# Kernel tuning notes

Measured on AMD Instinct MI355X. Metric: run time of the kernel, lower is better.

The kernel has to match this reference:

```python
import jax, jax.numpy as jnp
import numpy as np

N_ITEMS = 50000
N_USERS = 20000
N_NODES = N_ITEMS + N_USERS
D = 128
N_REL = 3
NNZ = 800000
K_LAYERS = 2
B, S, L = 256, 4, 50


def setup_inputs() -> dict:
    key = jax.random.key(0)
    ks = iter(jax.random.split(key, 40))
    stdv = float(1.0 / np.sqrt(D))

    def uni(shape):
        return jax.random.uniform(next(ks), shape, jnp.float32, -stdv, stdv)

    id_emb = (jax.random.normal(next(ks), (N_ITEMS, D), jnp.float32) * 0.1).at[0].set(0.0)  # padding_idx=0
    user_emb = jax.random.normal(next(ks), (N_USERS, D), jnp.float32) * 0.1
    inp = dict(
        id_emb=id_emb, user_emb=user_emb,
        lin_r_w=uni((K_LAYERS, N_REL, D, D)),
        upi_w=uni((K_LAYERS, D, D)), upi_b=uni((K_LAYERS, D)),
        upu_w=uni((K_LAYERS, D, D)), upu_b=uni((K_LAYERS, D)),
        w_ih=uni((3 * D, 2 * D)), w_hh=uni((3 * D, D)),
        b_ih=uni((3 * D,)), b_hh=uni((3 * D,)),
        b_iah=uni((D,)), b_oah=uni((D,)),
        ei_w=uni((D, D)), ei_b=uni((D,)),
        eo_w=uni((D, D)), eo_b=uni((D,)),
        q1_w=uni((D, D)), q2_w=uni((D, D)), att_w=uni((D,)),
        fuse_w=uni((D, 2 * D)), fuse_b=uni((D,)),
    )
    # global heterogeneous graph: COO per relation over item+user nodes
    inp['rel_rows'] = jax.random.randint(next(ks), (N_REL, NNZ), 0, N_NODES, dtype=jnp.int32)
    inp['rel_cols'] = jax.random.randint(next(ks), (N_REL, NNZ), 0, N_NODES, dtype=jnp.int32)
    inp['rel_vals'] = jax.random.uniform(next(ks), (N_REL, NNZ), jnp.float32) * 0.1
    # session batch: every session has length in [2, L]
    lens = jax.random.randint(next(ks), (B, S), 2, L + 1)
    raw = jax.random.randint(next(ks), (B, S, L), 1, N_ITEMS)
    inp['ids'] = (raw * (jnp.arange(L)[None, None, :] < lens[:, :, None])).astype(jnp.int32)
    inp['uid'] = jax.random.randint(next(ks), (B,), 0, N_USERS, dtype=jnp.int32)
    inp['u_type'] = jax.random.randint(next(ks), (B,), 0, 3).astype(jnp.float32)
    return inp


def _hgnn(h_item, h_user, rel_rows, rel_cols, rel_vals, lin_r_w, upi_w, upi_b, upu_w, upu_b):
    Ni = h_item.shape[0]
    N = Ni + h_user.shape[0]
    for k in range(lin_r_w.shape[0]):
        h_all = jnp.concatenate([h_item, h_user], 0)
        msg = jnp.zeros_like(h_all)
        for r in range(rel_rows.shape[0]):
            Wh = h_all @ lin_r_w[k, r].T  # per-relation linear
            msg = msg + jax.ops.segment_sum(Wh[rel_cols[r]] * rel_vals[r][:, None],
                                            rel_rows[r], num_segments=N)  # sparse.mm
        h_item = jax.nn.relu((msg[:Ni] + h_item) @ upi_w[k].T + upi_b[k])
        h_user = jax.nn.relu((msg[Ni:] + h_user) @ upu_w[k].T + upu_b[k])
    return h_item, h_user


def reference(id_emb, user_emb, lin_r_w, upi_w, upi_b, upu_w, upu_b,
              w_ih, w_hh, b_ih, b_hh, b_iah, b_oah,
              ei_w, ei_b, eo_w, eo_b, q1_w, q2_w, att_w, fuse_w, fuse_b,
              rel_rows, rel_cols, rel_vals, ids, uid, u_type):
    Bb, Ss, Ll = ids.shape
    N = Ss * Bb
    ids_sb = jnp.transpose(ids, (1, 0, 2)).reshape(N, Ll)  # session-major, matches torch concat order
    lens = (ids_sb != 0).sum(-1)  # >= 2 by construction -> all sessions valid
    rows = jnp.arange(N)
    target = ids_sb[rows, lens - 1]
    Lp = Ll - 1
    m_in = jnp.arange(Lp)[None, :] < (lens - 1)[:, None]
    seq_in = ids_sb[:, :Lp] * m_in
    # session graph: consecutive-item edges; in-half sub-diagonal, out-half super-diagonal
    valid = (m_in[:, 1:] & m_in[:, :-1]).astype(jnp.float32)  # [N, Lp-1]
    i1 = jnp.arange(1, Lp)
    i0 = jnp.arange(Lp - 1)
    a_in = jnp.zeros((N, Lp, Lp), jnp.float32).at[:, i1, i0].set(valid)
    a_out = jnp.zeros((N, Lp, Lp), jnp.float32).at[:, i0, i1].set(valid)
    deg = jnp.clip(a_in.sum(-1), 1.0, None)[..., None]
    a_in = a_in / deg
    a_out = a_out / deg
    h = id_emb[seq_in]  # [N, Lp, D]
    # SessionGNN GRU-style cell (step=1)
    m_i = jnp.matmul(a_in, h @ ei_w.T + ei_b) + b_iah
    m_o = jnp.matmul(a_out, h @ eo_w.T + eo_b) + b_oah
    gi = jnp.concatenate([m_i, m_o], -1) @ w_ih.T + b_ih
    gh = h @ w_hh.T + b_hh
    i_r, i_i, i_n = jnp.split(gi, 3, -1)
    h_r, h_i, h_n = jnp.split(gh, 3, -1)
    rg = jax.nn.sigmoid(i_r + h_r)
    zg = jax.nn.sigmoid(i_i + h_i)
    ng = jnp.tanh(i_n + rg * h_n)
    h = ng + zg * (h - ng)
    # attention readout
    ht = h[rows, jnp.clip(lens - 2, 0, None)]
    alpha = jax.nn.sigmoid((ht @ q1_w.T)[:, None, :] + h @ q2_w.T) @ att_w  # [N, Lp]
    alpha = alpha * m_in.astype(jnp.float32)
    alpha = alpha / (alpha.sum(1, keepdims=True) + 1e-8)
    c_cur = jnp.einsum('nl,nld->nd', alpha, h)
    # global HGNN user context
    g_item, g_user = _hgnn(id_emb[:N_ITEMS], user_emb[:N_USERS], rel_rows, rel_cols,
                           rel_vals, lin_r_w, upi_w, upi_b, upu_w, upu_b)
    c_hist = g_user[jnp.tile(uid, Ss)]
    reps = jnp.concatenate([c_cur, c_hist], -1) @ fuse_w.T + fuse_b
    return reps, target, jnp.tile(u_type, Ss)
```

## Files before the change

### kernel.cpp

```cpp
#include <hip/hip_runtime.h>
#include <hip/hip_bf16.h>

typedef __hip_bfloat16 bf16;
typedef unsigned int uint32;
typedef __attribute__((ext_vector_type(8))) short short8;
typedef __attribute__((ext_vector_type(4))) float f32x4;

#define N_ITEMS_C 50000
#define N_USERS_C 20000
#define N_NODES_C 70000
#define NNZ_C 800000
#define NSESS 1024
#define LP 49
#define NTOK (NSESS * LP)
#define NBK 137

__device__ __forceinline__ float bflo(uint32 u) { return __uint_as_float(u << 16); }
__device__ __forceinline__ float bfhi(uint32 u) { return __uint_as_float(u & 0xffff0000u); }
__device__ __forceinline__ uint32 packbf(float a, float b) {
    return (uint32)__bfloat16_as_ushort(__float2bfloat16(a)) |
           ((uint32)__bfloat16_as_ushort(__float2bfloat16(b)) << 16);
}

__global__ void init_hab_kernel(const float2* __restrict__ idp, const float2* __restrict__ usp,
                                uint32* __restrict__ hab) {
    int i = blockIdx.x * 256 + threadIdx.x;
    float2 w = (i < 3200000) ? idp[i] : usp[i - 3200000];
    hab[i] = packbf(w.x, w.y);
}

__global__ __launch_bounds__(256) void bucket_hist_kernel(
    const int* __restrict__ rel_rows, int* __restrict__ bhist)
{
    __shared__ int hist[NBK];
    const int r = blockIdx.y, tid = threadIdx.x;
    if (tid < NBK) hist[tid] = 0;
    __syncthreads();
    const int* rr = rel_rows + (size_t)r * NNZ_C;
#pragma unroll
    for (int i = 0; i < 16; ++i) {
        int e = blockIdx.x * 4096 + i * 256 + tid;
        if (e < NNZ_C) atomicAdd(&hist[rr[e] >> 9], 1);
    }
    __syncthreads();
    if (tid < NBK && hist[tid]) atomicAdd(&bhist[r * NBK + tid], hist[tid]);
}

__global__ __launch_bounds__(256) void bucket_scan_kernel(
    const int* __restrict__ bhist, int* __restrict__ bbase)
{
    __shared__ int s[256];
    const int tid = threadIdx.x;
    for (int r = 0; r < 3; ++r) {
        s[tid] = (tid < NBK) ? bhist[r * NBK + tid] : 0;
        __syncthreads();
        for (int d = 1; d < 256; d <<= 1) {
            int t = (tid >= d) ? s[tid - d] : 0;
            __syncthreads();
            s[tid] += t;
            __syncthreads();
        }
        if (tid < NBK) bbase[r * (NBK + 1) + tid + 1] = s[tid];
        if (tid == 0) bbase[r * (NBK + 1)] = 0;
        __syncthreads();
    }
}

__global__ __launch_bounds__(256) void bucket_scatter_kernel(
    const int* __restrict__ rel_rows, const int* __restrict__ rel_cols,
    const float* __restrict__ rel_vals, const int* __restrict__ bbase,
    int* __restrict__ cursor, int2* __restrict__ tmp)
{
    __shared__ int hist[NBK], gbase[NBK], cur2[NBK];
    const int r = blockIdx.y, tid = threadIdx.x;
    if (tid < NBK) { hist[tid] = 0; cur2[tid] = 0; }
    __syncthreads();
    const int* rr = rel_rows + (size_t)r * NNZ_C;
    const int* rc = rel_cols + (size_t)r * NNZ_C;
    const float* rv = rel_vals + (size_t)r * NNZ_C;
#pragma unroll
    for (int i = 0; i < 16; ++i) {
        int e = blockIdx.x * 4096 + i * 256 + tid;
        if (e < NNZ_C) atomicAdd(&hist[rr[e] >> 9], 1);
    }
    __syncthreads();
    if (tid < NBK)
        gbase[tid] = bbase[r * (NBK + 1) + tid] +
                     (hist[tid] ? atomicAdd(&cursor[r * NBK + tid], hist[tid]) : 0);
    __syncthreads();
    int2* tp = tmp + (size_t)r * NNZ_C;
#pragma unroll
    for (int i = 0; i < 16; ++i) {
        int e = blockIdx.x * 4096 + i * 256 + tid;
        if (e < NNZ_C) {
            int row = rr[e];
            int bk = row >> 9;
            int rank = atomicAdd(&cur2[bk], 1);
            uint32 fb = __float_as_uint(rv[e]);
            uint32 pk = (uint32)rc[e] | (((fb >> 16) & 0x7FFFu) << 17);
            tp[gbase[bk] + rank] = make_int2((int)pk, row);
        }
    }
}

__global__ __launch_bounds__(256) void bucket_refine_kernel(
    const int2* __restrict__ tmp, const int* __restrict__ bbase,
    int* __restrict__ offs, uint32* __restrict__ edges)
{
    __shared__ int cnt[512], offsL[512], cur[512];
    __shared__ uint32 outb[6656];
    const int b = blockIdx.x, r = blockIdx.y, tid = threadIdx.x;
    const int lane = tid & 63, wid = tid >> 6;
    const int row0 = b << 9;
    const int e0 = bbase[r * (NBK + 1) + b];
    const int e1 = bbase[r * (NBK + 1) + b + 1];
    cnt[tid] = 0; cnt[256 + tid] = 0; cur[tid] = 0; cur[256 + tid] = 0;
    __syncthreads();
    const int2* tp = tmp + (size_t)r * NNZ_C;
    for (int e = e0 + tid; e < e1; e += 256)
        atomicAdd(&cnt[tp[e].y - row0], 1);
    __syncthreads();
    if (wid == 0) {
        int carry = 0;
        for (int c = 0; c < 8; ++c) {
            int x = cnt[c * 64 + lane];
            int inc = x;
#pragma unroll
            for (int d = 1; d < 64; d <<= 1) {
                int y = __shfl_up(inc, d, 64);
                if (lane >= d) inc += y;
            }
            offsL[c * 64 + lane] = inc - x + carry;
            carry += __shfl(inc, 63, 64);
        }
    }
    __syncthreads();
    for (int i = tid; i < 512; i += 256) {
        int row = row0 + i;
        if (row < 70001) offs[(size_t)r * 70001 + row] = e0 + offsL[i];
    }
    for (int e = e0 + tid; e < e1; e += 256) {
        int2 E = tp[e];
        int lr_ = E.y - row0;
        int slot = offsL[lr_] + atomicAdd(&cur[lr_], 1);
        if (slot < 6656) outb[slot] = (uint32)E.x;
    }
    __syncthreads();
    uint32* eo = edges + (size_t)r * NNZ_C + e0;
    for (int i = tid; i < e1 - e0; i += 256) eo[i] = outb[i];
}

__global__ __launch_bounds__(256) void gather_kernel(
    const uint32* __restrict__ hab, const uint32* __restrict__ edges,
    const int* __restrict__ offs, uint32* __restrict__ T)
{
    const int r = blockIdx.y;
    const int row = blockIdx.x * 4 + (threadIdx.x >> 6);
    const int lane = threadIdx.x & 63;
    const uint32* __restrict__ ed = edges + (size_t)r * NNZ_C;
    const int* __restrict__ of = offs + (size_t)r * 70001;
    int e0 = of[row], e1 = of[row + 1];
    float ax = 0.f, ay = 0.f;
    int e = e0;
    for (; e + 4 <= e1; e += 4) {
        uint32 E0 = ed[e], E1 = ed[e + 1], E2 = ed[e + 2], E3 = ed[e + 3];
        uint32 u0 = hab[(size_t)(E0 & 0x1FFFFu) * 64 + lane];
        uint32 u1 = hab[(size_t)(E1 & 0x1FFFFu) * 64 + lane];
        uint32 u2 = hab[(size_t)(E2 & 0x1FFFFu) * 64 + lane];
        uint32 u3 = hab[(size_t)(E3 & 0x1FFFFu) * 64 + lane];
        float v0 = __uint_as_float((E0 >> 1) & 0x7FFF0000u);
        float v1 = __uint_as_float((E1 >> 1) & 0x7FFF0000u);
        float v2 = __uint_as_float((E2 >> 1) & 0x7FFF0000u);
        float v3 = __uint_as_float((E3 >> 1) & 0x7FFF0000u);
        ax += v0 * bflo(u0) + v1 * bflo(u1) + v2 * bflo(u2) + v3 * bflo(u3);
        ay += v0 * bfhi(u0) + v1 * bfhi(u1) + v2 * bfhi(u2) + v3 * bfhi(u3);
    }
    for (; e < e1; ++e) {
        uint32 E = ed[e];
        uint32 u = hab[(size_t)(E & 0x1FFFFu) * 64 + lane];
        float v = __uint_as_float((E >> 1) & 0x7FFF0000u);
        ax += v * bflo(u); ay += v * bfhi(u);
    }
    T[(size_t)row * 192 + r * 64 + lane] = packbf(ax, ay);
}

__global__ __launch_bounds__(256, 3) void wprep_kernel(
    const float* __restrict__ upi_w, const float* __restrict__ upu_w,
    const float* __restrict__ lin_r_w, int k, uint32* __restrict__ Wcat)
{
    __shared__ float As[128][65];
    __shared__ __align__(8) bf16 Ws[128][66];
    const int which = blockIdx.y, seg = which / 3, r = which % 3;
    const float* U  = (seg == 0 ? upi_w : upu_w) + (size_t)k * 16384;
    const float* Wr = lin_r_w + (size_t)(k * 3 + r) * 16384;
    uint32* out = Wcat + (size_t)seg * 32768;
    const int tid = threadIdx.x;
    const int row0 = blockIdx.x * 64;
#pragma unroll
    for (int i = 0; i < 8; ++i) {
        int id = i * 256 + tid;
        int rr = id >> 5, c4 = (id & 31) << 2;
        float4 v = *(const float4*)&U[(size_t)(row0 + rr) * 128 + c4];
        As[c4][rr] = v.x; As[c4+1][rr] = v.y; As[c4+2][rr] = v.z; As[c4+3][rr] = v.w;
    }
    const int m0 = (tid & 15) * 4;
    const int n0 = (tid >> 4) * 8;
    float acc[4][8];
#pragma unroll
    for (int i = 0; i < 4; ++i)
#pragma unroll
        for (int j = 0; j < 8; ++j) acc[i][j] = 0.f;
    for (int p = 0; p < 2; ++p) {
        if (p) __syncthreads();
        for (int i = 0; i < 32; ++i) {
            int id = i * 256 + tid;
            int c = id >> 6, kf = id & 63;
            Ws[c][kf] = __float2bfloat16(Wr[(size_t)(p * 64 + kf) * 128 + c]);
        }
        __syncthreads();
        for (int k2 = 0; k2 < 32; ++k2) {
            int kk = p * 64 + 2 * k2;
            float av0[4], av1[4];
#pragma unroll
            for (int i = 0; i < 4; ++i) { av0[i] = As[kk][m0 + i]; av1[i] = As[kk + 1][m0 + i]; }
#pragma unroll
            for (int j = 0; j < 8; ++j) {
                uint32 wp = *(const uint32*)&Ws[n0 + j][2 * k2];
                float w0 = bflo(wp), w1 = bfhi(wp);
#pragma unroll
                for (int i = 0; i < 4; ++i)
                    acc[i][j] = fmaf(av1[i], w1, fmaf(av0[i], w0, acc[i][j]));
            }
        }
    }
#pragma unroll
    for (int i = 0; i < 4; ++i) {
        int n = row0 + m0 + i;
#pragma unroll
        for (int j = 0; j < 8; j += 2)
            out[(size_t)n * 256 + (r * 128 + n0 + j) / 2] = packbf(acc[i][j], acc[i][j + 1]);
    }
}

__global__ __launch_bounds__(256) void upack_kernel(
    const float* __restrict__ upi_w, const float* __restrict__ upu_w,
    int k, uint32* __restrict__ Wcat)
{
    int id = blockIdx.x * 256 + threadIdx.x;
    int seg = id >> 13, p = id & 8191;
    int n = p >> 6, j2 = (p & 63);
    const float* U = (seg ? upu_w : upi_w) + (size_t)k * 16384;
    float2 w = *(const float2*)&U[(size_t)n * 128 + j2 * 2];
    Wcat[(size_t)seg * 32768 + (size_t)n * 256 + 192 + j2] = packbf(w.x, w.y);
}

__global__ __launch_bounds__(256) void hgnn_update_mfma_kernel(
    const bf16* __restrict__ T, uint32* __restrict__ hab,
    const bf16* __restrict__ Wcat, const float* __restrict__ bias, int row0, int M)
{
    const int tid = threadIdx.x;
    const int wv = tid >> 6, lane = tid & 63, quad = lane >> 4, lr = lane & 15;
    const int rbase = blockIdx.x * 64;
    const bf16* hb = (const bf16*)hab;
    f32x4 acc[4][2];
#pragma unroll
    for (int mt = 0; mt < 4; ++mt) { acc[mt][0] = (f32x4){0,0,0,0}; acc[mt][1] = (f32x4){0,0,0,0}; }
    int arow[4];
#pragma unroll
    for (int mt = 0; mt < 4; ++mt) {
        int rr = rbase + mt * 16 + lr;
        arow[mt] = row0 + (rr < M ? rr : M - 1);
    }
#pragma unroll
    for (int ks = 0; ks < 16; ++ks) {
        short8 b0 = *(const short8*)&Wcat[(size_t)(wv * 32 + lr) * 512 + ks * 32 + quad * 8];
        short8 b1 = *(const short8*)&Wcat[(size_t)(wv * 32 + 16 + lr) * 512 + ks * 32 + quad * 8];
#pragma unroll
        for (int mt = 0; mt < 4; ++mt) {
            short8 a;
            if (ks < 12) a = *(const short8*)&T[(size_t)arow[mt] * 384 + ks * 32 + quad * 8];
            else         a = *(const short8*)&hb[(size_t)arow[mt] * 128 + (ks - 12) * 32 + quad * 8];
            acc[mt][0] = __builtin_amdgcn_mfma_f32_16x16x32_bf16(a, b0, acc[mt][0], 0, 0, 0);
            acc[mt][1] = __builtin_amdgcn_mfma_f32_16x16x32_bf16(a, b1, acc[mt][1], 0, 0, 0);
        }
    }
    __syncthreads();
    unsigned short* hw = (unsigned short*)hab;
#pragma unroll
    for (int s = 0; s < 2; ++s) {
        int col = wv * 32 + s * 16 + lr;
        float bv = bias[col];
#pragma unroll
        for (int mt = 0; mt < 4; ++mt)
#pragma unroll
            for (int reg = 0; reg < 4; ++reg) {
                int rr = rbase + mt * 16 + quad * 4 + reg;
                if (rr < M) {
                    float v = fmaxf(acc[mt][s][reg] + bv, 0.f);
                    hw[(size_t)(row0 + rr) * 128 + col] = __bfloat16_as_ushort(__float2bfloat16(v));
                }
            }
    }
}

__global__ __launch_bounds__(256) void mfma_nt_kernel(
    const bf16* __restrict__ A, const int* __restrict__ rowmap,
    const bf16* __restrict__ W0, const bf16* __restrict__ W1,
    const float* __restrict__ b0, const float* __restrict__ b1,
    float* __restrict__ O0, float* __restrict__ O1, int M)
{
    const int tid = threadIdx.x;
    const int wv = tid >> 6, lane = tid & 63, quad = lane >> 4, lr = lane & 15;
    const int rbase = blockIdx.x * 64;
    int arow[4];
#pragma unroll
    for (int mt = 0; mt < 4; ++mt) {
        int rr = rbase + mt * 16 + lr;
        rr = rr < M ? rr : M - 1;
        arow[mt] = rowmap ? rowmap[rr] : rr;
    }
    f32x4 acc0[4][2], acc1[4][2];
#pragma unroll
    for (int mt = 0; mt < 4; ++mt) {
        acc0[mt][0] = (f32x4){0,0,0,0}; acc0[mt][1] = (f32x4){0,0,0,0};
        acc1[mt][0] = (f32x4){0,0,0,0}; acc1[mt][1] = (f32x4){0,0,0,0};
    }
#pragma unroll
    for (int ks = 0; ks < 4; ++ks) {
        short8 b00 = *(const short8*)&W0[(size_t)(wv * 32 + lr) * 128 + ks * 32 + quad * 8];
        short8 b01 = *(const short8*)&W0[(size_t)(wv * 32 + 16 + lr) * 128 + ks * 32 + quad * 8];
        short8 b10, b11;
        if (W1) {
            b10 = *(const short8*)&W1[(size_t)(wv * 32 + lr) * 128 + ks * 32 + quad * 8];
            b11 = *(const short8*)&W1[(size_t)(wv * 32 + 16 + lr) * 128 + ks * 32 + quad * 8];
        }
#pragma unroll
        for (int mt = 0; mt < 4; ++mt) {
            short8 a = *(const short8*)&A[(size_t)arow[mt] * 128 + ks * 32 + quad * 8];
            acc0[mt][0] = __builtin_amdgcn_mfma_f32_16x16x32_bf16(a, b00, acc0[mt][0], 0, 0, 0);
            acc0[mt][1] = __builtin_amdgcn_mfma_f32_16x16x32_bf16(a, b01, acc0[mt][1], 0, 0, 0);
            if (W1) {
                acc1[mt][0] = __builtin_amdgcn_mfma_f32_16x16x32_bf16(a, b10, acc1[mt][0], 0, 0, 0);
                acc1[mt][1] = __builtin_amdgcn_mfma_f32_16x16x32_bf16(a, b11, acc1[mt][1], 0, 0, 0);
            }
        }
    }
#pragma unroll
    for (int s = 0; s < 2; ++s) {
        int col = wv * 32 + s * 16 + lr;
        float bv0 = b0 ? b0[col] : 0.f;
        float bv1 = (W1 && b1) ? b1[col] : 0.f;
#pragma unroll
        for (int mt = 0; mt < 4; ++mt)
#pragma unroll
            for (int reg = 0; reg < 4; ++reg) {
                int rr = rbase + mt * 16 + quad * 4 + reg;
                if (rr < M) {
                    O0[(size_t)rr * 128 + col] = acc0[mt][s][reg] + bv0;
                    if (W1) O1[(size_t)rr * 128 + col] = acc1[mt][s][reg] + bv1;
                }
            }
    }
}

__global__ void session_prep_kernel(const int* __restrict__ ids, const int* __restrict__ uid,
                                    const float* __restrict__ u_type,
                                    int* __restrict__ lens, int* __restrict__ rowmap,
                                    float* __restrict__ out_target, float* __restrict__ out_utype)
{
    int n = blockIdx.x * 256 + threadIdx.x;
    if (n >= NSESS) return;
    int b = n & 255, s = n >> 8;
    const int* row = ids + (size_t)(b * 4 + s) * 50;
    int len = 0;
#pragma unroll
    for (int l = 0; l < 50; ++l) len += (row[l] != 0) ? 1 : 0;
    lens[n] = len;
    rowmap[n] = n * LP + (len - 2);
    out_target[n] = (float)row[len - 1];
    out_utype[n] = u_type[b];
}

__global__ void chist_kernel(const uint32* __restrict__ hab, const int* __restrict__ uid,
                             float* __restrict__ chist) {
    int n = blockIdx.x, d = threadIdx.x;
    uint32 u = hab[(size_t)(N_ITEMS_C + uid[n & 255]) * 64 + (d >> 1)];
    chist[(size_t)n * 128 + d] = (d & 1) ? bfhi(u) : bflo(u);
}

__global__ void h0_gather_kernel(const float* __restrict__ id_emb, const int* __restrict__ ids,
                                 const int* __restrict__ lens, uint32* __restrict__ hb) {
    int g = blockIdx.x, d = threadIdx.x;
    int n = g / LP;
    int tt = g - n * LP;
    int len = lens[n];
    int b = n & 255, s = n >> 8;
    int id = (tt < len - 1) ? ids[(size_t)(b * 4 + s) * 50 + tt] : 0;
    float2 e = *(const float2*)&id_emb[(size_t)id * 128 + d * 2];
    hb[(size_t)g * 64 + d] = packbf(e.x, e.y);
}

__global__ __launch_bounds__(256) void epack_kernel(
    const float* __restrict__ w_ih, const float* __restrict__ w_hh,
    const float* __restrict__ ei_w, const float* __restrict__ eo_w,
    const float* __restrict__ q2_w, const float* __restrict__ q1_w,
    uint32* __restrict__ dst)
{
    int id = blockIdx.x * 256 + threadIdx.x;
    const float* src; int off;
    if      (id <  49152) { src = w_ih; off = id; }
    else if (id <  73728) { src = w_hh; off = id - 49152; }
    else if (id <  81920) { src = ei_w; off = id - 73728; }
    else if (id <  90112) { src = eo_w; off = id - 81920; }
    else if (id <  98304) { src = q2_w; off = id - 90112; }
    else                  { src = q1_w; off = id - 98304; }
    float2 w = *(const float2*)&src[(size_t)off * 2];
    dst[id] = packbf(w.x, w.y);
}

__global__ __launch_bounds__(256, 2) void gru_mfma_kernel(
    const float* __restrict__ hEi, const float* __restrict__ hEo,
    uint32* __restrict__ hb, const int* __restrict__ lens,
    const bf16* __restrict__ wihb,
    const bf16* __restrict__ whhb,
    const float* __restrict__ b_ih, const float* __restrict__ b_hh,
    const float* __restrict__ b_iah, const float* __restrict__ b_oah)
{
    __shared__ __align__(16) bf16 Agi[16][264];
    __shared__ __align__(16) bf16 Agh[16][136];
    const int tid = threadIdx.x;
    const int g0 = blockIdx.x * 16;

#pragma unroll
    for (int i = 0; i < 8; ++i) {
        int p = i * 256 + tid;
        int row = p >> 7, kp = p & 127;
        int g = g0 + row;
        int n = g / LP;
        int tt = g - n * LP;
        int len = lens[n];
        int kk = (kp & 63) * 2;
        float v0, v1;
        if (kp < 64) {
            v0 = b_iah[kk]; v1 = b_iah[kk + 1];
            if (tt >= 1 && tt < len - 1) {
                float2 e = *(const float2*)&hEi[(size_t)(g - 1) * 128 + kk];
                v0 += e.x; v1 += e.y;
            }
        } else {
            v0 = b_oah[kk]; v1 = b_oah[kk + 1];
            if (tt < len - 2) {
                float2 e = *(const float2*)&hEo[(size_t)(g + 1) * 128 + kk];
                v0 += e.x; v1 += e.y;
            }
        }
        *(uint32*)&Agi[row][kp * 2] = packbf(v0, v1);
    }
#pragma unroll
    for (int i = 0; i < 4; ++i) {
        int p = i * 256 + tid;
        int row = p >> 6, kp = p & 63;
        *(uint32*)&Agh[row][kp * 2] = hb[(size_t)(g0 + row) * 64 + kp];
    }
    __syncthreads();

    const int wv = tid >> 6;
    const int lane = tid & 63;
    const int quad = lane >> 4;
    const int lr = lane & 15;
    const int c0 = wv * 32;

    f32x4 accI[2][3], accH[2][3];
#pragma unroll
    for (int s = 0; s < 2; ++s)
#pragma unroll
        for (int gte = 0; gte < 3; ++gte) {
            accI[s][gte] = (f32x4){0.f, 0.f, 0.f, 0.f};
            accH[s][gte] = (f32x4){0.f, 0.f, 0.f, 0.f};
        }

#pragma unroll
    for (int ks = 0; ks < 8; ++ks) {
        short8 a = *(const short8*)&Agi[lr][ks * 32 + quad * 8];
#pragma unroll
        for (int s = 0; s < 2; ++s)
#pragma unroll
            for (int gte = 0; gte < 3; ++gte) {
                int n0 = gte * 128 + c0 + s * 16 + lr;
                short8 b = *(const short8*)&wihb[(size_t)n0 * 256 + ks * 32 + quad * 8];
                accI[s][gte] = __builtin_amdgcn_mfma_f32_16x16x32_bf16(a, b, accI[s][gte], 0, 0, 0);
            }
    }
#pragma unroll
    for (int ks = 0; ks < 4; ++ks) {
        short8 a = *(const short8*)&Agh[lr][ks * 32 + quad * 8];
#pragma unroll
        for (int s = 0; s < 2; ++s)
#pragma unroll
            for (int gte = 0; gte < 3; ++gte) {
                int n0 = gte * 128 + c0 + s * 16 + lr;
                short8 b = *(const short8*)&whhb[(size_t)n0 * 128 + ks * 32 + quad * 8];
                accH[s][gte] = __builtin_amdgcn_mfma_f32_16x16x32_bf16(a, b, accH[s][gte], 0, 0, 0);
            }
    }

    unsigned short* hu = (unsigned short*)hb;
#pragma unroll
    for (int s = 0; s < 2; ++s) {
        int col = c0 + s * 16 + lr;
        float bir = b_ih[col], biz = b_ih[col + 128], bin = b_ih[col + 256];
        float bhr = b_hh[col], bhz = b_hh[col + 128], bhn = b_hh[col + 256];
#pragma unroll
        for (int reg = 0; reg < 4; ++reg) {
            int row = g0 + quad * 4 + reg;
            float gi_r = accI[s][0][reg] + bir, gh_r = accH[s][0][reg] + bhr;
            float gi_z = accI[s][1][reg] + biz, gh_z = accH[s][1][reg] + bhz;
            float gi_n = accI[s][2][reg] + bin, gh_n = accH[s][2][reg] + bhn;
            float rg = 1.f / (1.f + expf(-(gi_r + gh_r)));
            float zg = 1.f / (1.f + expf(-(gi_z + gh_z)));
            float ng = tanhf(gi_n + rg * gh_n);
            size_t idx = (size_t)row * 128 + col;
            float ho = __uint_as_float((uint32)hu[idx] << 16);
            hu[idx] = __bfloat16_as_ushort(__float2bfloat16(ng + zg * (ho - ng)));
        }
    }
}

__global__ __launch_bounds__(128) void attn_fuse_kernel(
    const float* __restrict__ q1h, const float* __restrict__ q2h,
    const unsigned short* __restrict__ hu, const float* __restrict__ chist,
    const int* __restrict__ lens, const float* __restrict__ att_w,
    const float* __restrict__ fuse_w, const float* __restrict__ fuse_b,
    float* __restrict__ out)
{
    __shared__ float q1s[128], aws[128], al[64], cv[256];
    const int n = blockIdx.x, tid = threadIdx.x;
    q1s[tid] = q1h[(size_t)n * 128 + tid];
    aws[tid] = att_w[tid];
    if (tid < 64) al[tid] = 0.f;
    __syncthreads();
    const int len = lens[n];
    if (tid < len - 1) {
        const float* q2 = &q2h[(size_t)(n * LP + tid) * 128];
        float s = 0.f;
        for (int d = 0; d < 128; ++d) {
            float x = q1s[d] + q2[d];
            s += aws[d] / (1.f + expf(-x));
        }
        al[tid] = s;
    }
    __syncthreads();
    float ssum = 0.f;
    for (int t = 0; t < len - 1; ++t) ssum += al[t];
    float inv = 1.f / (ssum + 1e-8f);
    float c = 0.f;
    for (int t = 0; t < len - 1; ++t) {
        float hv = __uint_as_float((uint32)hu[(size_t)(n * LP + t) * 128 + tid] << 16);
        c += al[t] * inv * hv;
    }
    cv[tid] = c;
    cv[128 + tid] = chist[(size_t)n * 128 + tid];
    __syncthreads();
    float s = fuse_b[tid];
    const float* fr = fuse_w + (size_t)tid * 256;
    for (int k = 0; k < 256; ++k) s += cv[k] * fr[k];
    out[(size_t)n * 128 + tid] = s;
}

extern "C" void kernel_launch(void* const* d_in, const int* in_sizes, int n_in,
                              void* d_out, int out_size, void* d_ws, size_t ws_size,
                              hipStream_t stream)
{
    const float* id_emb   = (const float*)d_in[0];
    const float* user_emb = (const float*)d_in[1];
    const float* lin_r_w  = (const float*)d_in[2];
    const float* upi_w    = (const float*)d_in[3];
    const float* upi_b    = (const float*)d_in[4];
    const float* upu_w    = (const float*)d_in[5];
    const float* upu_b    = (const float*)d_in[6];
    const float* w_ih     = (const float*)d_in[7];
    const float* w_hh     = (const float*)d_in[8];
    const float* b_ih     = (const float*)d_in[9];
    const float* b_hh     = (const float*)d_in[10];
    const float* b_iah    = (const float*)d_in[11];
    const float* b_oah    = (const float*)d_in[12];
    const float* ei_w     = (const float*)d_in[13];
    const float* ei_b     = (const float*)d_in[14];
    const float* eo_w     = (const float*)d_in[15];
    const float* eo_b     = (const float*)d_in[16];
    const float* q1_w     = (const float*)d_in[17];
    const float* q2_w     = (const float*)d_in[18];
    const float* att_w    = (const float*)d_in[19];
    const float* fuse_w   = (const float*)d_in[20];
    const float* fuse_b   = (const float*)d_in[21];
    const int*  rel_rows  = (const int*)d_in[22];
    const int*  rel_cols  = (const int*)d_in[23];
    const float* rel_vals = (const float*)d_in[24];
    const int*  ids       = (const int*)d_in[25];
    const int*  uid       = (const int*)d_in[26];
    const float* u_type   = (const float*)d_in[27];
    float* out = (float*)d_out;

    uint32* W32    = (uint32*)d_ws;
    uint32* hab    = W32;
    uint32* T      = W32 + 4480000;
    uint32* edges  = W32 + 17920000;
    int2*   tmp    = (int2*)(W32 + 20320000);
    int*    offs   = (int*)(W32 + 25120000);
    int*    bhist  = (int*)(W32 + 25330004);
    int*    cursor = (int*)(W32 + 25330415);
    int*    bbase  = (int*)(W32 + 25330826);
    uint32* Wcat   = W32 + 25331240;
    float*  q1h    = (float*)(W32 + 25396776);
    float*  chist  = (float*)(W32 + 25527848);
    int*    lens   = (int*)(W32 + 25658920);
    int*    rowmap = (int*)(W32 + 25659944);
    uint32* sess_hb = W32;
    float* sess_Ei  = (float*)(W32 + 4480000);
    float* sess_Eo  = (float*)(W32 + 10902528);
    float* q2h      = sess_Ei;
    uint32* wpk     = W32 + 17920000;
    uint32* wihb = wpk;
    uint32* whhb = wpk + 49152;
    uint32* eiwb = wpk + 73728;
    uint32* eowb = wpk + 81920;
    uint32* q2wb = wpk + 90112;
    uint32* q1wb = wpk + 98304;
    if (ws_size < (size_t)27144192 * 4 + 4096) return;

    init_hab_kernel<<<17500, 256, 0, stream>>>((const float2*)id_emb, (const float2*)user_emb, hab);
    hipMemsetAsync(bhist, 0, (size_t)822 * 4, stream);
    bucket_hist_kernel<<<dim3(196, 3), 256, 0, stream>>>(rel_rows, bhist);
    bucket_scan_kernel<<<1, 256, 0, stream>>>(bhist, bbase);
    bucket_scatter_kernel<<<dim3(196, 3), 256, 0, stream>>>(rel_rows, rel_cols, rel_vals,
                                                            bbase, cursor, tmp);
    bucket_refine_kernel<<<dim3(NBK, 3), 256, 0, stream>>>(tmp, bbase, offs, edges);

    for (int k = 0; k < 2; ++k) {
        wprep_kernel<<<dim3(2, 6), 256, 0, stream>>>(upi_w, upu_w, lin_r_w, k, Wcat);
        upack_kernel<<<64, 256, 0, stream>>>(upi_w, upu_w, k, Wcat);
        gather_kernel<<<dim3(17500, 3), 256, 0, stream>>>(hab, edges, offs, T);
        hgnn_update_mfma_kernel<<<782, 256, 0, stream>>>((const bf16*)T, hab,
            (const bf16*)Wcat, upi_b + k * 128, 0, N_ITEMS_C);
        hgnn_update_mfma_kernel<<<313, 256, 0, stream>>>((const bf16*)T, hab,
            (const bf16*)(Wcat + 32768), upu_b + k * 128, N_ITEMS_C, N_USERS_C);
    }

    session_prep_kernel<<<4, 256, 0, stream>>>(ids, uid, u_type, lens, rowmap,
        out + 131072, out + 132096);
    chist_kernel<<<NSESS, 128, 0, stream>>>(hab, uid, chist);
    epack_kernel<<<416, 256, 0, stream>>>(w_ih, w_hh, ei_w, eo_w, q2_w, q1_w, wpk);
    h0_gather_kernel<<<NTOK, 64, 0, stream>>>(id_emb, ids, lens, sess_hb);
    mfma_nt_kernel<<<784, 256, 0, stream>>>((const bf16*)sess_hb, nullptr,
        (const bf16*)eiwb, (const bf16*)eowb, ei_b, eo_b, sess_Ei, sess_Eo, NTOK);
    gru_mfma_kernel<<<NTOK / 16, 256, 0, stream>>>(sess_Ei, sess_Eo, sess_hb, lens,
        (const bf16*)wihb, (const bf16*)whhb, b_ih, b_hh, b_iah, b_oah);
    mfma_nt_kernel<<<784, 256, 0, stream>>>((const bf16*)sess_hb, nullptr,
        (const bf16*)q2wb, nullptr, nullptr, nullptr, q2h, nullptr, NTOK);
    mfma_nt_kernel<<<16, 256, 0, stream>>>((const bf16*)sess_hb, rowmap,
        (const bf16*)q1wb, nullptr, nullptr, nullptr, q1h, nullptr, NSESS);
    attn_fuse_kernel<<<NSESS, 128, 0, stream>>>(q1h, q2h, (const unsigned short*)sess_hb,
        chist, lens, att_w, fuse_w, fuse_b, out);
}
```

Baseline: 870.0 us.

## Tile GRU kernel over 64 tokens per block to reuse weight fragments

Grows the GRU MFMA kernel's row tile from 16 to 64 tokens per block, so each B-fragment load of w_ih/w_hh from global memory is reused across four M-tiles instead of one. This cuts global weight traffic per token by about four times. The r and z gate accumulators for the input and hidden paths are now merged into shared accumulators, with the biases summed up front. The cost is more accumulator registers (32 f32x4 per thread), four times the LDS per block, and a quarter as many blocks, which may reduce occupancy under launch_bounds(256,2).

New measurement: 825.9 us. -5.1%, faster.

```diff
diff --git a/kernel.cpp b/kernel.cpp
--- a/kernel.cpp
+++ b/kernel.cpp
@@ -426,13 +426,13 @@
     const float* __restrict__ b_ih, const float* __restrict__ b_hh,
     const float* __restrict__ b_iah, const float* __restrict__ b_oah)
 {
-    __shared__ __align__(16) bf16 Agi[16][264];
-    __shared__ __align__(16) bf16 Agh[16][136];
+    __shared__ __align__(16) bf16 Agi[64][264];
+    __shared__ __align__(16) bf16 Agh[64][136];
     const int tid = threadIdx.x;
-    const int g0 = blockIdx.x * 16;
-
-#pragma unroll
-    for (int i = 0; i < 8; ++i) {
+    const int g0 = blockIdx.x * 64;
+
+#pragma unroll 4
+    for (int i = 0; i < 32; ++i) {
         int p = i * 256 + tid;
         int row = p >> 7, kp = p & 127;
         int g = g0 + row;
@@ -456,8 +456,8 @@
         }
         *(uint32*)&Agi[row][kp * 2] = packbf(v0, v1);
     }
-#pragma unroll
-    for (int i = 0; i < 4; ++i) {
+#pragma unroll 4
+    for (int i = 0; i < 16; ++i) {
         int p = i * 256 + tid;
         int row = p >> 6, kp = p & 63;
         *(uint32*)&Agh[row][kp * 2] = hb[(size_t)(g0 + row) * 64 + kp];
@@ -470,59 +470,77 @@
     const int lr = lane & 15;
     const int c0 = wv * 32;
 
-    f32x4 accI[2][3], accH[2][3];
-#pragma unroll
-    for (int s = 0; s < 2; ++s)
-#pragma unroll
-        for (int gte = 0; gte < 3; ++gte) {
-            accI[s][gte] = (f32x4){0.f, 0.f, 0.f, 0.f};
-            accH[s][gte] = (f32x4){0.f, 0.f, 0.f, 0.f};
-        }
-
-#pragma unroll
+    f32x4 acc[4][2][4];
+#pragma unroll
+    for (int mt = 0; mt < 4; ++mt)
+#pragma unroll
+        for (int s = 0; s < 2; ++s)
+#pragma unroll
+            for (int j = 0; j < 4; ++j) acc[mt][s][j] = (f32x4){0.f, 0.f, 0.f, 0.f};
+
+#pragma unroll 2
     for (int ks = 0; ks < 8; ++ks) {
-        short8 a = *(const short8*)&Agi[lr][ks * 32 + quad * 8];
+        short8 bfr[2][3];
 #pragma unroll
         for (int s = 0; s < 2; ++s)
 #pragma unroll
             for (int gte = 0; gte < 3; ++gte) {
                 int n0 = gte * 128 + c0 + s * 16 + lr;
-                short8 b = *(const short8*)&wihb[(size_t)n0 * 256 + ks * 32 + quad * 8];
-                accI[s][gte] = __builtin_amdgcn_mfma_f32_16x16x32_bf16(a, b, accI[s][gte], 0, 0, 0);
-            }
-    }
-#pragma unroll
+                bfr[s][gte] = *(const short8*)&wihb[(size_t)n0 * 256 + ks * 32 + quad * 8];
+            }
+#pragma unroll
+        for (int mt = 0; mt < 4; ++mt) {
+            short8 a = *(const short8*)&Agi[mt * 16 + lr][ks * 32 + quad * 8];
+#pragma unroll
+            for (int s = 0; s < 2; ++s) {
+                acc[mt][s][0] = __builtin_amdgcn_mfma_f32_16x16x32_bf16(a, bfr[s][0], acc[mt][s][0], 0, 0, 0);
+                acc[mt][s][1] = __builtin_amdgcn_mfma_f32_16x16x32_bf16(a, bfr[s][1], acc[mt][s][1], 0, 0, 0);
+                acc[mt][s][2] = __builtin_amdgcn_mfma_f32_16x16x32_bf16(a, bfr[s][2], acc[mt][s][2], 0, 0, 0);
+            }
+        }
+    }
+#pragma unroll 2
     for (int ks = 0; ks < 4; ++ks) {
-        short8 a = *(const short8*)&Agh[lr][ks * 32 + quad * 8];
+        short8 bfr[2][3];
 #pragma unroll
         for (int s = 0; s < 2; ++s)
 #pragma unroll
             for (int gte = 0; gte < 3; ++gte) {
                 int n0 = gte * 128 + c0 + s * 16 + lr;
-                short8 b = *(const short8*)&whhb[(size_t)n0 * 128 + ks * 32 + quad * 8];
-                accH[s][gte] = __builtin_amdgcn_mfma_f32_16x16x32_bf16(a, b, accH[s][gte], 0, 0, 0);
-            }
+                bfr[s][gte] = *(const short8*)&whhb[(size_t)n0 * 128 + ks * 32 + quad * 8];
+            }
+#pragma unroll
+        for (int mt = 0; mt < 4; ++mt) {
+            short8 a = *(const short8*)&Agh[mt * 16 + lr][ks * 32 + quad * 8];
+#pragma unroll
+            for (int s = 0; s < 2; ++s) {
+                acc[mt][s][0] = __builtin_amdgcn_mfma_f32_16x16x32_bf16(a, bfr[s][0], acc[mt][s][0], 0, 0, 0);
+                acc[mt][s][1] = __builtin_amdgcn_mfma_f32_16x16x32_bf16(a, bfr[s][1], acc[mt][s][1], 0, 0, 0);
+                acc[mt][s][3] = __builtin_amdgcn_mfma_f32_16x16x32_bf16(a, bfr[s][2], acc[mt][s][3], 0, 0, 0);
+            }
+        }
     }
 
     unsigned short* hu = (unsigned short*)hb;
 #pragma unroll
     for (int s = 0; s < 2; ++s) {
         int col = c0 + s * 16 + lr;
-        float bir = b_ih[col], biz = b_ih[col + 128], bin = b_ih[col + 256];
-        float bhr = b_hh[col], bhz = b_hh[col + 128], bhn = b_hh[col + 256];
-#pragma unroll
-        for (int reg = 0; reg < 4; ++reg) {
-            int row = g0 + quad * 4 + reg;
-            float gi_r = accI[s][0][reg] + bir, gh_r = accH[s][0][reg] + bhr;
-            float gi_z = accI[s][1][reg] + biz, gh_z = accH[s][1][reg] + bhz;
-            float gi_n = accI[s][2][reg] + bin, gh_n = accH[s][2][reg] + bhn;
-            float rg = 1.f / (1.f + expf(-(gi_r + gh_r)));
-            float zg = 1.f / (1.f + expf(-(gi_z + gh_z)));
-            float ng = tanhf(gi_n + rg * gh_n);
-            size_t idx = (size_t)row * 128 + col;
-            float ho = __uint_as_float((uint32)hu[idx] << 16);
-            hu[idx] = __bfloat16_as_ushort(__float2bfloat16(ng + zg * (ho - ng)));
-        }
+        float brz = b_ih[col] + b_hh[col];
+        float bzz = b_ih[col + 128] + b_hh[col + 128];
+        float bin = b_ih[col + 256];
+        float bhn = b_hh[col + 256];
+#pragma unroll
+        for (int mt = 0; mt < 4; ++mt)
+#pragma unroll
+            for (int reg = 0; reg < 4; ++reg) {
+                int row = g0 + mt * 16 + quad * 4 + reg;
+                float rg = 1.f / (1.f + expf(-(acc[mt][s][0][reg] + brz)));
+                float zg = 1.f / (1.f + expf(-(acc[mt][s][1][reg] + bzz)));
+                float ng = tanhf(acc[mt][s][2][reg] + bin + rg * (acc[mt][s][3][reg] + bhn));
+                size_t idx = (size_t)row * 128 + col;
+                float ho = __uint_as_float((uint32)hu[idx] << 16);
+                hu[idx] = __bfloat16_as_ushort(__float2bfloat16(ng + zg * (ho - ng)));
+            }
     }
 }
 
@@ -653,7 +671,7 @@
     h0_gather_kernel<<<NTOK, 64, 0, stream>>>(id_emb, ids, lens, sess_hb);
     mfma_nt_kernel<<<784, 256, 0, stream>>>((const bf16*)sess_hb, nullptr,
         (const bf16*)eiwb, (const bf16*)eowb, ei_b, eo_b, sess_Ei, sess_Eo, NTOK);
-    gru_mfma_kernel<<<NTOK / 16, 256, 0, stream>>>(sess_Ei, sess_Eo, sess_hb, lens,
+    gru_mfma_kernel<<<NTOK / 64, 256, 0, stream>>>(sess_Ei, sess_Eo, sess_hb, lens,
         (const bf16*)wihb, (const bf16*)whhb, b_ih, b_hh, b_iah, b_oah);
     mfma_nt_kernel<<<784, 256, 0, stream>>>((const bf16*)sess_hb, nullptr,
         (const bf16*)q2wb, nullptr, nullptr, nullptr, q2h, nullptr, NTOK);
```
